# Performance work log

Measured on AMD Instinct MI355X. Metric: run time of the kernel, lower is better.

The kernel has to match this reference:

```python
import jax, jax.numpy as jnp
import numpy as np

D_MODEL = 256
NUM_HEADS = 8
DEPTH = D_MODEL // NUM_HEADS
CITY_SEQ = 2048
B = 4
SQ = 2048
EPS = 1e-9
WEIGHTING = 'IDW'  # branch used (Linear/IDW/Gaussian in original)


def setup_inputs() -> dict:
    key = jax.random.key(0)
    ks = jax.random.split(key, 12)
    s = 1.0 / np.sqrt(D_MODEL)
    return {
        'query': jax.random.normal(ks[0], (B, SQ, D_MODEL), jnp.float32),
        'values': jax.random.normal(ks[1], (B, SQ, D_MODEL), jnp.float32),
        'distance_matrix': jax.random.uniform(ks[2], (B, SQ, CITY_SEQ), jnp.float32),
        'Wq_w': jax.random.normal(ks[3], (D_MODEL, D_MODEL), jnp.float32) * s,
        'Wq_b': jnp.zeros((D_MODEL,), jnp.float32),
        'Wk_w': jax.random.normal(ks[4], (D_MODEL, D_MODEL), jnp.float32) * s,
        'Wk_b': jnp.zeros((D_MODEL,), jnp.float32),
        'Wv_w': jax.random.normal(ks[5], (D_MODEL, D_MODEL), jnp.float32) * s,
        'Wv_b': jnp.zeros((D_MODEL,), jnp.float32),
        'fc_w': jax.random.normal(ks[6], (D_MODEL, D_MODEL), jnp.float32) * s,
        'fc_b': jnp.zeros((D_MODEL,), jnp.float32),
        'trainable_keys': jax.random.normal(ks[7], (CITY_SEQ, D_MODEL), jnp.float32),
    }


def _distance_weights(dist):
    # IDW branch: per-row normalized inverse distance, shape [B, Sq, S]
    inv = 1.0 / (dist + EPS)
    return inv / jnp.sum(inv, axis=-1, keepdims=True)


def reference(query, values, distance_matrix, Wq_w, Wq_b, Wk_w, Wk_b,
              Wv_w, Wv_b, fc_w, fc_b, trainable_keys):
    b = query.shape[0]
    q = query @ Wq_w.T + Wq_b                      # [B, Sq, D]
    k = trainable_keys @ Wk_w.T + Wk_b             # [S, D] (shared across batch)
    v = values @ Wv_w.T + Wv_b                     # [B, S, D]

    qh = q.reshape(b, -1, NUM_HEADS, DEPTH)        # [B, Sq, H, d]
    kh = k.reshape(-1, NUM_HEADS, DEPTH)           # [S, H, d]
    vh = v.reshape(b, -1, NUM_HEADS, DEPTH)        # [B, S, H, d]

    scale = 1.0 / jnp.sqrt(jnp.asarray(DEPTH, jnp.float32))
    scores = jnp.einsum('bqhd,khd->bhqk', qh, kh) * scale   # [B, H, Sq, S]
    dw = _distance_weights(distance_matrix)[:, None, :, :]  # [B, 1, Sq, S]
    scores = scores * dw
    attn = jax.nn.softmax(scores, axis=-1)
    out = jnp.einsum('bhqk,bkhd->bqhd', attn, vh).reshape(b, -1, D_MODEL)
    return out @ fc_w.T + fc_b
```

## Files before the change

kernel.cpp:

```cpp
#include <hip/hip_runtime.h>

#define BB 4
#define SQn 2048
#define SS 2048
#define DM 256
#define DH 32

typedef unsigned short u16;
typedef unsigned int u32;
typedef _Float16 f16;
typedef __attribute__((ext_vector_type(8))) f16 f16x8;
typedef __attribute__((ext_vector_type(4))) f16 f16x4;
typedef __attribute__((ext_vector_type(8))) short s16x8;
typedef __attribute__((ext_vector_type(4))) float f32x4;
typedef __attribute__((ext_vector_type(2))) float f32x2;
typedef __attribute__((ext_vector_type(4))) u32 u32x4;
typedef __attribute__((ext_vector_type(2))) u32 u32x2;

__device__ __forceinline__ float bf2f(u16 x){ u32 u=((u32)x)<<16; return __builtin_bit_cast(float,u); }
__device__ __forceinline__ u16 f2bf(float f){ u32 u=__builtin_bit_cast(u32,f); u32 r=(u+0x7fffu+((u>>16)&1u))>>16; return (u16)r; }

__device__ __forceinline__ f16x8 ld8(const void* p, size_t off, int fl)
{
    f16x8 r;
    if (fl) {
        const float* f = (const float*)p + off;
        f32x4 a = *(const f32x4*)f;
        f32x4 b = *(const f32x4*)(f + 4);
        #pragma unroll
        for (int i = 0; i < 4; ++i) { r[i] = (f16)a[i]; r[4+i] = (f16)b[i]; }
    } else {
        const u16* s = (const u16*)p + off;
        u32x4 v = *(const u32x4*)s;
        #pragma unroll
        for (int i = 0; i < 4; ++i) {
            u32 x = v[i];
            r[2*i]   = (f16)bf2f((u16)(x & 0xffff));
            r[2*i+1] = (f16)bf2f((u16)(x >> 16));
        }
    }
    return r;
}
__device__ __forceinline__ float ld1(const void* p, int idx, int fl)
{ return fl ? ((const float*)p)[idx] : bf2f(((const u16*)p)[idx]); }

__global__ void detect_kernel(const u32* __restrict__ q, int* __restrict__ flag)
{
    int t = threadIdx.x;
    u32 w = q[t];
    u32 e = (w >> 7) & 0xFFu;
    int vote = ((e >= 0x70u && e <= 0x85u) || ((w & 0xFFFFu) == 0u)) ? 1 : 0;
    #pragma unroll
    for (int d = 1; d < 64; d <<= 1) vote += __shfl_xor(vote, d);
    __shared__ int ps[4];
    if ((t & 63) == 0) ps[t >> 6] = vote;
    __syncthreads();
    if (t == 0) *flag = ((ps[0]+ps[1]+ps[2]+ps[3]) >= 128) ? 0 : 1;
}

__global__ __launch_bounds__(256) void proj_kernel(
    const int* __restrict__ flag,
    const void* __restrict__ query, const void* __restrict__ values, const void* __restrict__ tkeys,
    const void* __restrict__ Wq, const void* __restrict__ Wqb,
    const void* __restrict__ Wk, const void* __restrict__ Wkb,
    const void* __restrict__ Wv, const void* __restrict__ Wvb,
    f16* __restrict__ qf, f16* __restrict__ kf, u16* __restrict__ vt)
{
    int fl = *flag;
    int bx = blockIdx.x;
    const void *X, *W, *Bi; int mode, rowbase;
    if (bx < 128)      { X=query;  W=Wq; Bi=Wqb; mode=0; rowbase=bx*64; }
    else if (bx < 256) { X=values; W=Wv; Bi=Wvb; mode=2; rowbase=(bx-128)*64; }
    else               { X=tkeys;  W=Wk; Bi=Wkb; mode=1; rowbase=(bx-256)*64; }
    int colbase = blockIdx.y * 64;

    __shared__ f16 Xs[64][40];
    __shared__ f16 Ws[64][40];
    __shared__ u16 Os[64][72];

    int t = threadIdx.x;
    int lane = t & 63, w = t >> 6;
    int quad = lane >> 4, l15 = lane & 15;

    const f32x4 fz = {0.f,0.f,0.f,0.f};
    f32x4 acc[4] = {fz,fz,fz,fz};

    for (int ks = 0; ks < 8; ++ks) {
        int k0 = ks * 32;
        {
            int row = t >> 2, ch = (t & 3) * 8;
            f16x8 xv = ld8(X, (size_t)(rowbase+row)*DM + k0 + ch, fl);
            f16x8 wv = ld8(W, (size_t)(colbase+row)*DM + k0 + ch, fl);
            *(f16x8*)(&Xs[row][ch]) = xv;
            *(f16x8*)(&Ws[row][ch]) = wv;
        }
        __syncthreads();
        f16x8 a = *(const f16x8*)(&Xs[w*16 + l15][quad*8]);
        #pragma unroll
        for (int nt = 0; nt < 4; ++nt) {
            f16x8 bfr = *(const f16x8*)(&Ws[nt*16 + l15][quad*8]);
            acc[nt] = __builtin_amdgcn_mfma_f32_16x16x32_f16(a, bfr, acc[nt], 0, 0, 0);
        }
        __syncthreads();
    }

    if (mode == 2) {
        int m = rowbase + w*16 + quad*4;
        int bb = m >> 11, s = m & 2047;
        int ktv = s >> 5, qv = (s >> 3) & 3, kk = s & 7;
        #pragma unroll
        for (int nt = 0; nt < 4; ++nt) {
            int col = colbase + nt*16 + l15;
            float bv = ld1(Bi, col, fl);
            int hv = col >> 5, ntv = (col >> 4) & 1;
            size_t idx = (((((size_t)(bb*8 + hv))*64 + ktv)*2 + ntv)*4 + qv)*128
                         + (size_t)(col & 15)*8 + kk;
            u32x2 pk;
            pk[0] = (u32)f2bf(acc[nt][0]+bv) | ((u32)f2bf(acc[nt][1]+bv) << 16);
            pk[1] = (u32)f2bf(acc[nt][2]+bv) | ((u32)f2bf(acc[nt][3]+bv) << 16);
            *(u32x2*)(vt + idx) = pk;
        }
    } else {
        #pragma unroll
        for (int nt = 0; nt < 4; ++nt) {
            int col = nt*16 + l15;
            float bv = ld1(Bi, colbase + col, fl);
            #pragma unroll
            for (int r = 0; r < 4; ++r)
                Os[w*16 + quad*4 + r][col] = __builtin_bit_cast(u16, (f16)(acc[nt][r] + bv));
        }
        __syncthreads();
        #pragma unroll
        for (int p = 0; p < 2; ++p) {
            int rr = (t >> 3) + p*32;
            int ch = (t & 7) * 8;
            u32x4 v = *(const u32x4*)(&Os[rr][ch]);
            if (mode == 0) {
                *(u32x4*)(qf + (size_t)(rowbase+rr)*DM + colbase + ch) = v;
            } else {
                int head = (colbase + ch) >> 5;
                int dh = ch & 31;
                *(u32x4*)(kf + (size_t)head*(SS*DH) + (size_t)(rowbase+rr)*DH + dh) = v;
            }
        }
    }
}

__global__ __launch_bounds__(256) void dwsum_kernel(
    const int* __restrict__ flag, const void* __restrict__ dist, u16* __restrict__ distT)
{
    int fl = *flag;
    int row = blockIdx.x;
    int t = threadIdx.x;

    float d[8];
    if (fl) {
        const float* p = (const float*)dist + (size_t)row * SS + t*8;
        f32x4 a = *(const f32x4*)p;
        f32x4 b4 = *(const f32x4*)(p + 4);
        #pragma unroll
        for (int i = 0; i < 4; ++i) { d[i] = a[i]; d[4+i] = b4[i]; }
    } else {
        const u16* p = (const u16*)dist + (size_t)row * SS + t*8;
        u32x4 v = *(const u32x4*)p;
        #pragma unroll
        for (int i = 0; i < 4; ++i) {
            u32 x = v[i];
            d[2*i]   = bf2f((u16)(x & 0xffff));
            d[2*i+1] = bf2f((u16)(x >> 16));
        }
    }
    float s = 0.f;
    #pragma unroll
    for (int i = 0; i < 8; ++i) s += 1.0f / (d[i] + 1e-9f);
    #pragma unroll
    for (int dd = 1; dd < 64; dd <<= 1) s += __shfl_xor(s, dd);
    __shared__ float ps[4];
    __shared__ float srs;
    if ((t & 63) == 0) ps[t >> 6] = s;
    __syncthreads();
    if (t == 0) srs = 0.17677669529663687f / (ps[0] + ps[1] + ps[2] + ps[3]);
    __syncthreads();
    float rs = srs;

    int b = row >> 11, q = row & 2047;
    int qt = q >> 5, ql = q & 31;
    size_t base = ((size_t)((b*64 + qt)*64 + (t >> 2)))*1024 + ql*32 + (t & 3)*8;
    u32x4 pk;
    #pragma unroll
    for (int i = 0; i < 4; ++i) {
        u16 lo = __builtin_bit_cast(u16, (f16)(rs * __builtin_amdgcn_rcpf(d[2*i]   + 1e-9f)));
        u16 hi = __builtin_bit_cast(u16, (f16)(rs * __builtin_amdgcn_rcpf(d[2*i+1] + 1e-9f)));
        pk[i] = (u32)lo | ((u32)hi << 16);
    }
    *(u32x4*)(distT + base) = pk;
}

#define LDP 40
#define LDO 264
#define DB_OFF 53248
#define OL_OFF  49152
#define OUTF_OFF 66048

__global__ __launch_bounds__(1024) void attn_kernel(
    const int* __restrict__ flag,
    const u16* __restrict__ distT,
    const f16* __restrict__ qf, const f16* __restrict__ kf, const u16* __restrict__ vtg,
    const void* __restrict__ fcw, const void* __restrict__ fcb,
    void* __restrict__ out)
{
    __shared__ __align__(16) char smem[99840];

    int fl = *flag;
    int t = threadIdx.x;
    int w = t >> 6, lane = t & 63;
    int quad = lane >> 4, l15 = lane & 15;
    int b = blockIdx.y, q0 = blockIdx.x * 32;
    int h = w & 7, khalf = w >> 3;

    u16* Pw = (u16*)(smem + w * 2560);
    u16* dbU = (u16*)(smem + DB_OFF);

    f16x8 aq[2];
    #pragma unroll
    for (int mt = 0; mt < 2; ++mt)
        aq[mt] = *(const f16x8*)(qf + (size_t)(b*SQn + q0 + mt*16 + l15)*DM + h*DH + quad*8);

    u32 ov = (l15 == 0) ? 0x3F803F80u : 0u;
    u32x4 ovv = {ov, ov, ov, ov};
    s16x8 ones = __builtin_bit_cast(s16x8, ovv);

    const f32x4 fz = {0.f,0.f,0.f,0.f};
    f32x4 o[2][2] = {{fz,fz},{fz,fz}};
    f32x4 lacc[2] = {fz, fz};

    const f16* kfh = kf + (size_t)h * (SS*DH);
    const u16* vth = vtg + (((size_t)(b*8 + h)) << 16);
    const u16* dTb = distT + ((size_t)(b*64 + blockIdx.x))*64*1024;

    int g  = t >> 9;
    int tt = t & 511;
    int drow = tt >> 4, dcol = (tt & 15)*2;

    {
        u32 sv = *(const u32*)(dTb + (size_t)(g*32)*1024 + tt*2);
        *(u32*)(dbU + g*1152 + drow*36 + dcol) = sv;
    }
    f16x8 ck[2]; s16x8 cv[2];
    {
        int ktg0 = khalf * 32;
        #pragma unroll
        for (int nt = 0; nt < 2; ++nt) {
            ck[nt] = *(const f16x8*)(kfh + (size_t)(ktg0*32 + nt*16 + l15)*DH + quad*8);
            cv[nt] = __builtin_bit_cast(s16x8,
                *(const u32x4*)(vth + (size_t)ktg0*1024 + nt*512 + quad*128 + l15*8));
        }
    }
    __syncthreads();

    for (int kt = 0; kt < 32; ++kt) {
        int ktn  = (kt + 1) & 31;
        int ktgn = khalf*32 + ktn;

        u32 sv = *(const u32*)(dTb + (size_t)(g*32 + ktn)*1024 + tt*2);
        f16x8 nk[2]; s16x8 nv[2];
        #pragma unroll
        for (int nt = 0; nt < 2; ++nt) {
            nk[nt] = *(const f16x8*)(kfh + (size_t)(ktgn*32 + nt*16 + l15)*DH + quad*8);
            nv[nt] = __builtin_bit_cast(s16x8,
                *(const u32x4*)(vth + (size_t)ktgn*1024 + nt*512 + quad*128 + l15*8));
        }

        const u16* dbc = dbU + ((kt & 1)*2 + khalf)*1152;
        f16x4 ddh[2][2];
        #pragma unroll
        for (int mt = 0; mt < 2; ++mt)
            #pragma unroll
            for (int nt = 0; nt < 2; ++nt)
                ddh[mt][nt] = *(const f16x4*)(dbc + (mt*16 + l15)*36 + nt*16 + quad*4);

        f32x4 st[2][2];
        #pragma unroll
        for (int mt = 0; mt < 2; ++mt)
            #pragma unroll
            for (int nt = 0; nt < 2; ++nt)
                st[mt][nt] = __builtin_amdgcn_mfma_f32_16x16x32_f16(ck[nt], aq[mt], fz, 0, 0, 0);

        #pragma unroll
        for (int mt = 0; mt < 2; ++mt)
            #pragma unroll
            for (int nt = 0; nt < 2; ++nt) {
                u32 pb[4];
                #pragma unroll
                for (int r = 0; r < 4; ++r) {
                    float p = __expf(st[mt][nt][r] * (float)ddh[mt][nt][r]);
                    pb[r] = __builtin_bit_cast(u32, p);
                }
                u32x2 pk;
                pk[0] = __builtin_amdgcn_perm(pb[1], pb[0], 0x07060302u);
                pk[1] = __builtin_amdgcn_perm(pb[3], pb[2], 0x07060302u);
                *(u32x2*)(Pw + (mt*16 + l15)*LDP + nt*16 + quad*4) = pk;
            }
        __asm__ __volatile__("" ::: "memory");

        #pragma unroll
        for (int mt = 0; mt < 2; ++mt) {
            s16x8 ap = *(const s16x8*)(Pw + (mt*16 + l15)*LDP + quad*8);
            lacc[mt] = __builtin_amdgcn_mfma_f32_16x16x32_bf16(ap, ones, lacc[mt], 0, 0, 0);
            #pragma unroll
            for (int nt = 0; nt < 2; ++nt)
                o[mt][nt] = __builtin_amdgcn_mfma_f32_16x16x32_bf16(ap, cv[nt], o[mt][nt], 0, 0, 0);
        }

        *(u32*)(dbU + (((kt + 1) & 1)*2 + g)*1152 + drow*36 + dcol) = sv;
        __syncthreads();

        ck[0] = nk[0]; ck[1] = nk[1]; cv[0] = nv[0]; cv[1] = nv[1];
    }

    float* Cx = (float*)smem;
    if (w >= 8) {
        float* dst = Cx + ((w - 8)*64 + lane)*24;
        *(f32x4*)(dst +  0) = o[0][0];
        *(f32x4*)(dst +  4) = o[0][1];
        *(f32x4*)(dst +  8) = o[1][0];
        *(f32x4*)(dst + 12) = o[1][1];
        *(f32x4*)(dst + 16) = lacc[0];
        *(f32x4*)(dst + 20) = lacc[1];
    }
    __syncthreads();
    f16* Ol = (f16*)(smem + OL_OFF);
    if (w < 8) {
        const float* src = Cx + (w*64 + lane)*24;
        o[0][0] += *(const f32x4*)(src +  0);
        o[0][1] += *(const f32x4*)(src +  4);
        o[1][0] += *(const f32x4*)(src +  8);
        o[1][1] += *(const f32x4*)(src + 12);
        lacc[0] += *(const f32x4*)(src + 16);
        lacc[1] += *(const f32x4*)(src + 20);

        #pragma unroll
        for (int mt = 0; mt < 2; ++mt)
            #pragma unroll
            for (int r = 0; r < 4; ++r) {
                float lv = __shfl(lacc[mt][r], lane & 48);
                float inv = 1.0f / lv;
                o[mt][0][r] *= inv;
                o[mt][1][r] *= inv;
            }

        #pragma unroll
        for (int mt = 0; mt < 2; ++mt)
            #pragma unroll
            for (int nt = 0; nt < 2; ++nt)
                #pragma unroll
                for (int r = 0; r < 4; ++r)
                    Ol[(mt*16 + quad*4 + r)*LDO + h*DH + nt*16 + l15] = (f16)o[mt][nt][r];
    }
    __syncthreads();

    f32x4 c[2] = {fz, fz};
    int n = w*16 + l15;
    for (int ks = 0; ks < 8; ++ks) {
        f16x8 bw = ld8(fcw, (size_t)n*DM + ks*32 + quad*8, fl);
        #pragma unroll
        for (int mt = 0; mt < 2; ++mt) {
            f16x8 a2 = *(const f16x8*)(Ol + (mt*16 + l15)*LDO + ks*32 + quad*8);
            c[mt] = __builtin_amdgcn_mfma_f32_16x16x32_f16(a2, bw, c[mt], 0, 0, 0);
        }
    }
    float* OutF = (float*)(smem + OUTF_OFF);
    {
        float bv = ld1(fcb, n, fl);
        #pragma unroll
        for (int mt = 0; mt < 2; ++mt)
            #pragma unroll
            for (int r = 0; r < 4; ++r)
                OutF[(mt*16 + quad*4 + r)*LDO + n] = c[mt][r] + bv;
    }
    __syncthreads();
    if (fl) {
        float* of = (float*)out;
        int row = t >> 5, col = (t & 31) * 8;
        f32x4 v0 = *(const f32x4*)(OutF + row*LDO + col);
        f32x4 v1 = *(const f32x4*)(OutF + row*LDO + col + 4);
        float* dst = of + ((size_t)(b*SQn + q0 + row))*DM + col;
        *(f32x4*)dst       = v0;
        *(f32x4*)(dst + 4) = v1;
    } else {
        u16* ob = (u16*)out;
        int row = t >> 5, col = (t & 31) * 8;
        f32x4 v0 = *(const f32x4*)(OutF + row*LDO + col);
        f32x4 v1 = *(const f32x4*)(OutF + row*LDO + col + 4);
        u32x4 pk;
        pk[0] = (u32)f2bf(v0[0]) | ((u32)f2bf(v0[1]) << 16);
        pk[1] = (u32)f2bf(v0[2]) | ((u32)f2bf(v0[3]) << 16);
        pk[2] = (u32)f2bf(v1[0]) | ((u32)f2bf(v1[1]) << 16);
        pk[3] = (u32)f2bf(v1[2]) | ((u32)f2bf(v1[3]) << 16);
        *(u32x4*)(ob + ((size_t)(b*SQn + q0 + row))*DM + col) = pk;
    }
}

extern "C" void kernel_launch(void* const* d_in, const int* in_sizes, int n_in,
                              void* d_out, int out_size, void* d_ws, size_t ws_size,
                              hipStream_t stream)
{
    const void* query  = d_in[0];
    const void* values = d_in[1];
    const void* dist   = d_in[2];
    const void* Wq     = d_in[3];
    const void* Wqb    = d_in[4];
    const void* Wk     = d_in[5];
    const void* Wkb    = d_in[6];
    const void* Wv     = d_in[7];
    const void* Wvb    = d_in[8];
    const void* fcw    = d_in[9];
    const void* fcb    = d_in[10];
    const void* tkeys  = d_in[11];

    char* ws   = (char*)d_ws;
    f16*  qf   = (f16*)ws;
    f16*  kf   = (f16*)(ws + (4u << 20));
    u16*  vt   = (u16*)(ws + (5u << 20));
    int*  flag = (int*)(ws + (9u << 20));
    u16*  dT   = (u16*)(ws + (16u << 20));

    detect_kernel<<<1, 256, 0, stream>>>((const u32*)query, flag);
    proj_kernel<<<dim3(288, 4), 256, 0, stream>>>(flag, query, values, tkeys,
                                                  Wq, Wqb, Wk, Wkb, Wv, Wvb,
                                                  qf, kf, vt);
    dwsum_kernel<<<dim3(BB * SQn), 256, 0, stream>>>(flag, dist, dT);
    attn_kernel<<<dim3(64, 4), 1024, 0, stream>>>(flag, dT, qf, kf, vt, fcw, fcb, d_out);
}
```

Measured before the change: 194.0 us.

## Merge detect, projection and distance-weight kernels into one launch

Removes the separate dtype-detect kernel by recomputing the flag per block with a wavefront ballot over 64 words. Projection and distance-normalisation kernels become a single launch with block-index dispatch, so they can run concurrently and two launch gaps disappear. The costs are a shared-memory footprint sized for the larger branch and redundant detection loads in every block. The detection now samples 64 words instead of 256, which could change the result on borderline inputs.

```diff
diff --git a/kernel.cpp b/kernel.cpp
--- a/kernel.cpp
+++ b/kernel.cpp
@@ -20,6 +20,15 @@
 __device__ __forceinline__ float bf2f(u16 x){ u32 u=((u32)x)<<16; return __builtin_bit_cast(float,u); }
 __device__ __forceinline__ u16 f2bf(float f){ u32 u=__builtin_bit_cast(u32,f); u32 r=(u+0x7fffu+((u>>16)&1u))>>16; return (u16)r; }
 
+__device__ __forceinline__ int detect_fl(const u32* __restrict__ q)
+{
+    u32 w = q[threadIdx.x & 63];
+    u32 e = (w >> 7) & 0xFFu;
+    int v = ((e >= 0x70u && e <= 0x85u) || ((w & 0xFFFFu) == 0u)) ? 1 : 0;
+    unsigned long long b = __ballot(v);
+    return (__popcll(b) >= 32) ? 0 : 1;
+}
+
 __device__ __forceinline__ f16x8 ld8(const void* p, size_t off, int fl)
 {
     f16x8 r;
@@ -44,156 +53,142 @@
 __device__ __forceinline__ float ld1(const void* p, int idx, int fl)
 { return fl ? ((const float*)p)[idx] : bf2f(((const u16*)p)[idx]); }
 
-__global__ void detect_kernel(const u32* __restrict__ q, int* __restrict__ flag)
-{
-    int t = threadIdx.x;
-    u32 w = q[t];
-    u32 e = (w >> 7) & 0xFFu;
-    int vote = ((e >= 0x70u && e <= 0x85u) || ((w & 0xFFFFu) == 0u)) ? 1 : 0;
-    #pragma unroll
-    for (int d = 1; d < 64; d <<= 1) vote += __shfl_xor(vote, d);
-    __shared__ int ps[4];
-    if ((t & 63) == 0) ps[t >> 6] = vote;
-    __syncthreads();
-    if (t == 0) *flag = ((ps[0]+ps[1]+ps[2]+ps[3]) >= 128) ? 0 : 1;
-}
-
-__global__ __launch_bounds__(256) void proj_kernel(
-    const int* __restrict__ flag,
+__global__ __launch_bounds__(256) void mega_kernel(
     const void* __restrict__ query, const void* __restrict__ values, const void* __restrict__ tkeys,
     const void* __restrict__ Wq, const void* __restrict__ Wqb,
     const void* __restrict__ Wk, const void* __restrict__ Wkb,
     const void* __restrict__ Wv, const void* __restrict__ Wvb,
-    f16* __restrict__ qf, f16* __restrict__ kf, u16* __restrict__ vt)
+    const void* __restrict__ dist,
+    f16* __restrict__ qf, f16* __restrict__ kf, u16* __restrict__ vt,
+    u16* __restrict__ distT)
 {
-    int fl = *flag;
-    int bx = blockIdx.x;
-    const void *X, *W, *Bi; int mode, rowbase;
-    if (bx < 128)      { X=query;  W=Wq; Bi=Wqb; mode=0; rowbase=bx*64; }
-    else if (bx < 256) { X=values; W=Wv; Bi=Wvb; mode=2; rowbase=(bx-128)*64; }
-    else               { X=tkeys;  W=Wk; Bi=Wkb; mode=1; rowbase=(bx-256)*64; }
-    int colbase = blockIdx.y * 64;
-
-    __shared__ f16 Xs[64][40];
-    __shared__ f16 Ws[64][40];
-    __shared__ u16 Os[64][72];
-
+    __shared__ __align__(16) char sm[19968];
+    int fl = detect_fl((const u32*)query);
+    int x = blockIdx.x;
     int t = threadIdx.x;
-    int lane = t & 63, w = t >> 6;
-    int quad = lane >> 4, l15 = lane & 15;
-
-    const f32x4 fz = {0.f,0.f,0.f,0.f};
-    f32x4 acc[4] = {fz,fz,fz,fz};
-
-    for (int ks = 0; ks < 8; ++ks) {
-        int k0 = ks * 32;
-        {
-            int row = t >> 2, ch = (t & 3) * 8;
-            f16x8 xv = ld8(X, (size_t)(rowbase+row)*DM + k0 + ch, fl);
-            f16x8 wv = ld8(W, (size_t)(colbase+row)*DM + k0 + ch, fl);
-            *(f16x8*)(&Xs[row][ch]) = xv;
-            *(f16x8*)(&Ws[row][ch]) = wv;
-        }
+
+    if (x < 1152) {
+        int pbx = x >> 2, pby = x & 3;
+        const void *X, *W, *Bi; int mode, rowbase;
+        if (pbx < 128)      { X=query;  W=Wq; Bi=Wqb; mode=0; rowbase=pbx*64; }
+        else if (pbx < 256) { X=values; W=Wv; Bi=Wvb; mode=2; rowbase=(pbx-128)*64; }
+        else                { X=tkeys;  W=Wk; Bi=Wkb; mode=1; rowbase=(pbx-256)*64; }
+        int colbase = pby * 64;
+
+        f16 (*Xs)[40] = (f16(*)[40])sm;
+        f16 (*Ws)[40] = (f16(*)[40])(sm + 5120);
+        u16 (*Os)[72] = (u16(*)[72])(sm + 10240);
+
+        int lane = t & 63, w = t >> 6;
+        int quad = lane >> 4, l15 = lane & 15;
+
+        const f32x4 fz = {0.f,0.f,0.f,0.f};
+        f32x4 acc[4] = {fz,fz,fz,fz};
+
+        for (int ks = 0; ks < 8; ++ks) {
+            int k0 = ks * 32;
+            {
+                int row = t >> 2, ch = (t & 3) * 8;
+                f16x8 xv = ld8(X, (size_t)(rowbase+row)*DM + k0 + ch, fl);
+                f16x8 wv = ld8(W, (size_t)(colbase+row)*DM + k0 + ch, fl);
+                *(f16x8*)(&Xs[row][ch]) = xv;
+                *(f16x8*)(&Ws[row][ch]) = wv;
+            }
+            __syncthreads();
+            f16x8 a = *(const f16x8*)(&Xs[w*16 + l15][quad*8]);
+            #pragma unroll
+            for (int nt = 0; nt < 4; ++nt) {
+                f16x8 bfr = *(const f16x8*)(&Ws[nt*16 + l15][quad*8]);
+                acc[nt] = __builtin_amdgcn_mfma_f32_16x16x32_f16(a, bfr, acc[nt], 0, 0, 0);
+            }
+            __syncthreads();
+        }
+
+        if (mode == 2) {
+            int m = rowbase + w*16 + quad*4;
+            int bb = m >> 11, s = m & 2047;
+            int ktv = s >> 5, qv = (s >> 3) & 3, kk = s & 7;
+            #pragma unroll
+            for (int nt = 0; nt < 4; ++nt) {
+                int col = colbase + nt*16 + l15;
+                float bv = ld1(Bi, col, fl);
+                int hv = col >> 5, ntv = (col >> 4) & 1;
+                size_t idx = (((((size_t)(bb*8 + hv))*64 + ktv)*2 + ntv)*4 + qv)*128
+                             + (size_t)(col & 15)*8 + kk;
+                u32x2 pk;
+                pk[0] = (u32)f2bf(acc[nt][0]+bv) | ((u32)f2bf(acc[nt][1]+bv) << 16);
+                pk[1] = (u32)f2bf(acc[nt][2]+bv) | ((u32)f2bf(acc[nt][3]+bv) << 16);
+                *(u32x2*)(vt + idx) = pk;
+            }
+        } else {
+            #pragma unroll
+            for (int nt = 0; nt < 4; ++nt) {
+                int col = nt*16 + l15;
+                float bv = ld1(Bi, colbase + col, fl);
+                #pragma unroll
+                for (int r = 0; r < 4; ++r)
+                    Os[w*16 + quad*4 + r][col] = __builtin_bit_cast(u16, (f16)(acc[nt][r] + bv));
+            }
+            __syncthreads();
+            #pragma unroll
+            for (int p = 0; p < 2; ++p) {
+                int rr = (t >> 3) + p*32;
+                int ch = (t & 7) * 8;
+                u32x4 v = *(const u32x4*)(&Os[rr][ch]);
+                if (mode == 0) {
+                    *(u32x4*)(qf + (size_t)(rowbase+rr)*DM + colbase + ch) = v;
+                } else {
+                    int head = (colbase + ch) >> 5;
+                    int dh = ch & 31;
+                    *(u32x4*)(kf + (size_t)head*(SS*DH) + (size_t)(rowbase+rr)*DH + dh) = v;
+                }
+            }
+        }
+    } else {
+        int row = x - 1152;
+        float* ps  = (float*)sm;
+        float* srs = (float*)(sm + 16);
+
+        float d[8];
+        if (fl) {
+            const float* p = (const float*)dist + (size_t)row * SS + t*8;
+            f32x4 a = *(const f32x4*)p;
+            f32x4 b4 = *(const f32x4*)(p + 4);
+            #pragma unroll
+            for (int i = 0; i < 4; ++i) { d[i] = a[i]; d[4+i] = b4[i]; }
+        } else {
+            const u16* p = (const u16*)dist + (size_t)row * SS + t*8;
+            u32x4 v = *(const u32x4*)p;
+            #pragma unroll
+            for (int i = 0; i < 4; ++i) {
+                u32 xw = v[i];
+                d[2*i]   = bf2f((u16)(xw & 0xffff));
+                d[2*i+1] = bf2f((u16)(xw >> 16));
+            }
+        }
+        float s = 0.f;
+        #pragma unroll
+        for (int i = 0; i < 8; ++i) s += 1.0f / (d[i] + 1e-9f);
+        #pragma unroll
+        for (int dd = 1; dd < 64; dd <<= 1) s += __shfl_xor(s, dd);
+        if ((t & 63) == 0) ps[t >> 6] = s;
         __syncthreads();
-        f16x8 a = *(const f16x8*)(&Xs[w*16 + l15][quad*8]);
-        #pragma unroll
-        for (int nt = 0; nt < 4; ++nt) {
-            f16x8 bfr = *(const f16x8*)(&Ws[nt*16 + l15][quad*8]);
-            acc[nt] = __builtin_amdgcn_mfma_f32_16x16x32_f16(a, bfr, acc[nt], 0, 0, 0);
-        }
+        if (t == 0) *srs = 0.17677669529663687f / (ps[0] + ps[1] + ps[2] + ps[3]);
         __syncthreads();
-    }
-
-    if (mode == 2) {
-        int m = rowbase + w*16 + quad*4;
-        int bb = m >> 11, s = m & 2047;
-        int ktv = s >> 5, qv = (s >> 3) & 3, kk = s & 7;
-        #pragma unroll
-        for (int nt = 0; nt < 4; ++nt) {
-            int col = colbase + nt*16 + l15;
-            float bv = ld1(Bi, col, fl);
-            int hv = col >> 5, ntv = (col >> 4) & 1;
-            size_t idx = (((((size_t)(bb*8 + hv))*64 + ktv)*2 + ntv)*4 + qv)*128
-                         + (size_t)(col & 15)*8 + kk;
-            u32x2 pk;
-            pk[0] = (u32)f2bf(acc[nt][0]+bv) | ((u32)f2bf(acc[nt][1]+bv) << 16);
-            pk[1] = (u32)f2bf(acc[nt][2]+bv) | ((u32)f2bf(acc[nt][3]+bv) << 16);
-            *(u32x2*)(vt + idx) = pk;
-        }
-    } else {
-        #pragma unroll
-        for (int nt = 0; nt < 4; ++nt) {
-            int col = nt*16 + l15;
-            float bv = ld1(Bi, colbase + col, fl);
-            #pragma unroll
-            for (int r = 0; r < 4; ++r)
-                Os[w*16 + quad*4 + r][col] = __builtin_bit_cast(u16, (f16)(acc[nt][r] + bv));
-        }
-        __syncthreads();
-        #pragma unroll
-        for (int p = 0; p < 2; ++p) {
-            int rr = (t >> 3) + p*32;
-            int ch = (t & 7) * 8;
-            u32x4 v = *(const u32x4*)(&Os[rr][ch]);
-            if (mode == 0) {
-                *(u32x4*)(qf + (size_t)(rowbase+rr)*DM + colbase + ch) = v;
-            } else {
-                int head = (colbase + ch) >> 5;
-                int dh = ch & 31;
-                *(u32x4*)(kf + (size_t)head*(SS*DH) + (size_t)(rowbase+rr)*DH + dh) = v;
-            }
-        }
-    }
-}
-
-__global__ __launch_bounds__(256) void dwsum_kernel(
-    const int* __restrict__ flag, const void* __restrict__ dist, u16* __restrict__ distT)
-{
-    int fl = *flag;
-    int row = blockIdx.x;
-    int t = threadIdx.x;
-
-    float d[8];
-    if (fl) {
-        const float* p = (const float*)dist + (size_t)row * SS + t*8;
-        f32x4 a = *(const f32x4*)p;
-        f32x4 b4 = *(const f32x4*)(p + 4);
-        #pragma unroll
-        for (int i = 0; i < 4; ++i) { d[i] = a[i]; d[4+i] = b4[i]; }
-    } else {
-        const u16* p = (const u16*)dist + (size_t)row * SS + t*8;
-        u32x4 v = *(const u32x4*)p;
+        float rs = *srs;
+
+        int b = row >> 11, q = row & 2047;
+        int qt = q >> 5, ql = q & 31;
+        size_t base = ((size_t)((b*64 + qt)*64 + (t >> 2)))*1024 + ql*32 + (t & 3)*8;
+        u32x4 pk;
         #pragma unroll
         for (int i = 0; i < 4; ++i) {
-            u32 x = v[i];
-            d[2*i]   = bf2f((u16)(x & 0xffff));
-            d[2*i+1] = bf2f((u16)(x >> 16));
-        }
-    }
-    float s = 0.f;
-    #pragma unroll
-    for (int i = 0; i < 8; ++i) s += 1.0f / (d[i] + 1e-9f);
-    #pragma unroll
-    for (int dd = 1; dd < 64; dd <<= 1) s += __shfl_xor(s, dd);
-    __shared__ float ps[4];
-    __shared__ float srs;
-    if ((t & 63) == 0) ps[t >> 6] = s;
-    __syncthreads();
-    if (t == 0) srs = 0.17677669529663687f / (ps[0] + ps[1] + ps[2] + ps[3]);
-    __syncthreads();
-    float rs = srs;
-
-    int b = row >> 11, q = row & 2047;
-    int qt = q >> 5, ql = q & 31;
-    size_t base = ((size_t)((b*64 + qt)*64 + (t >> 2)))*1024 + ql*32 + (t & 3)*8;
-    u32x4 pk;
-    #pragma unroll
-    for (int i = 0; i < 4; ++i) {
-        u16 lo = __builtin_bit_cast(u16, (f16)(rs * __builtin_amdgcn_rcpf(d[2*i]   + 1e-9f)));
-        u16 hi = __builtin_bit_cast(u16, (f16)(rs * __builtin_amdgcn_rcpf(d[2*i+1] + 1e-9f)));
-        pk[i] = (u32)lo | ((u32)hi << 16);
-    }
-    *(u32x4*)(distT + base) = pk;
+            u16 lo = __builtin_bit_cast(u16, (f16)(rs * __builtin_amdgcn_rcpf(d[2*i]   + 1e-9f)));
+            u16 hi = __builtin_bit_cast(u16, (f16)(rs * __builtin_amdgcn_rcpf(d[2*i+1] + 1e-9f)));
+            pk[i] = (u32)lo | ((u32)hi << 16);
+        }
+        *(u32x4*)(distT + base) = pk;
+    }
 }
 
 #define LDP 40
@@ -203,7 +198,7 @@
 #define OUTF_OFF 66048
 
 __global__ __launch_bounds__(1024) void attn_kernel(
-    const int* __restrict__ flag,
+    const void* __restrict__ queryp,
     const u16* __restrict__ distT,
     const f16* __restrict__ qf, const f16* __restrict__ kf, const u16* __restrict__ vtg,
     const void* __restrict__ fcw, const void* __restrict__ fcb,
@@ -211,7 +206,7 @@
 {
     __shared__ __align__(16) char smem[99840];
 
-    int fl = *flag;
+    int fl = detect_fl((const u32*)queryp);
     int t = threadIdx.x;
     int w = t >> 6, lane = t & 63;
     int quad = lane >> 4, l15 = lane & 15;
@@ -422,13 +417,9 @@
     f16*  qf   = (f16*)ws;
     f16*  kf   = (f16*)(ws + (4u << 20));
     u16*  vt   = (u16*)(ws + (5u << 20));
-    int*  flag = (int*)(ws + (9u << 20));
     u16*  dT   = (u16*)(ws + (16u << 20));
 
-    detect_kernel<<<1, 256, 0, stream>>>((const u32*)query, flag);
-    proj_kernel<<<dim3(288, 4), 256, 0, stream>>>(flag, query, values, tkeys,
-                                                  Wq, Wqb, Wk, Wkb, Wv, Wvb,
-                                                  qf, kf, vt);
-    dwsum_kernel<<<dim3(BB * SQn), 256, 0, stream>>>(flag, dist, dT);
-    attn_kernel<<<dim3(64, 4), 1024, 0, stream>>>(flag, dT, qf, kf, vt, fcw, fcb, d_out);
+    mega_kernel<<<dim3(1152 + BB*SQn), 256, 0, stream>>>(
+        query, values, tkeys, Wq, Wqb, Wk, Wkb, Wv, Wvb, dist, qf, kf, vt, dT);
+    attn_kernel<<<dim3(64, 4), 1024, 0, stream>>>(query, dT, qf, kf, vt, fcw, fcb, d_out);
 }
```

Result: no change. 191.7 us (-1.2%).
